# Performance work log

Hardware: AMD Instinct MI355X
Metric: run time of the kernel (lower is better)

The kernel has to match this reference:

```python
import jax, jax.numpy as jnp
import numpy as np

N = 32768          # total nodes
B = 64             # number of graphs (batch.max()+1)
IN_C = 256
OUT_C = 256
NUM_SCALES = 4
NUM_HEADS = 8
BN_EPS = 1e-5


def setup_inputs() -> dict:
    key = jax.random.key(0)
    ks = jax.random.split(key, 10)
    out_s = OUT_C // NUM_SCALES
    x = jax.random.normal(ks[0], (N, IN_C), jnp.float32)
    spectral = jax.random.normal(ks[1], (NUM_SCALES, N, IN_C), jnp.float32)
    batch = jnp.sort(jax.random.randint(ks[2], (N,), 0, B)).astype(jnp.int64)
    # per-scale Linear weights (glorot) and zero biases; stored as [S, in, out_s]
    g = (6.0 / (IN_C + out_s)) ** 0.5
    Ws = jax.random.uniform(ks[3], (NUM_SCALES, IN_C, out_s), jnp.float32, -g, g)
    bs = jnp.zeros((NUM_SCALES, out_s), jnp.float32)
    # MultiheadAttention params (torch layout: in_proj [3E,E], out_proj [E,E])
    s_in = (1.0 / OUT_C) ** 0.5
    W_in = jax.random.uniform(ks[4], (3 * OUT_C, OUT_C), jnp.float32, -s_in, s_in)
    b_in = jnp.zeros((3 * OUT_C,), jnp.float32)
    W_out = jax.random.uniform(ks[5], (OUT_C, OUT_C), jnp.float32, -s_in, s_in)
    b_out = jnp.zeros((OUT_C,), jnp.float32)
    gamma = jnp.ones((OUT_C,), jnp.float32)
    beta = jnp.zeros((OUT_C,), jnp.float32)
    return {"x": x, "spectral": spectral, "Ws": Ws, "bs": bs,
            "W_in": W_in, "b_in": b_in, "W_out": W_out, "b_out": b_out,
            "gamma": gamma, "beta": beta, "batch": batch}


def _forward(x, spectral, Ws, bs, W_in, b_in, W_out, b_out, gamma, beta, batch):
    n, E = x.shape[0], W_out.shape[0]
    # per-scale linear on (x + spectral_feat), concat over scales -> [N, E]
    scale_out = jnp.einsum('sni,sio->sno', x[None] + spectral, Ws) + bs[:, None, :]
    h = jnp.moveaxis(scale_out, 0, 1).reshape(n, E)
    # ragged -> dense padding (batch is sorted segment ids)
    counts = jnp.bincount(batch, length=B)
    max_nodes = int(np.asarray(counts).max())  # data-dependent pad, as in torch
    starts = jnp.concatenate([jnp.zeros((1,), counts.dtype), jnp.cumsum(counts)[:-1]])
    pos = jnp.arange(n) - starts[batch]
    h_pad = jnp.zeros((B, max_nodes, E), h.dtype).at[batch, pos].set(h)
    # MHA over padded graphs (no key-padding mask, matching the source)
    hd = E // NUM_HEADS
    qkv = h_pad @ W_in.T + b_in                       # [B, M, 3E]
    q, k, v = jnp.split(qkv, 3, axis=-1)
    def heads(t):
        return t.reshape(B, max_nodes, NUM_HEADS, hd).transpose(0, 2, 1, 3)
    q, k, v = heads(q) * (hd ** -0.5), heads(k), heads(v)
    attn = jax.nn.softmax(jnp.einsum('bhqd,bhkd->bhqk', q, k), axis=-1)
    ctx = jnp.einsum('bhqk,bhkd->bhqd', attn, v)
    ctx = ctx.transpose(0, 2, 1, 3).reshape(B, max_nodes, E)
    h_att = ctx @ W_out.T + b_out
    # dense -> ragged unpad
    h2 = h_att[batch, pos]                            # [N, E]
    # BatchNorm1d (training-mode batch stats, deterministic) + ReLU; dropout=eval
    mean = h2.mean(axis=0)
    var = h2.var(axis=0)
    hn = (h2 - mean) * jax.lax.rsqrt(var + BN_EPS) * gamma + beta
    return jax.nn.relu(hn)


def reference(x, spectral, Ws, bs, W_in, b_in, W_out, b_out, gamma, beta, batch):
    return _forward(x, spectral, Ws, bs, W_in, b_in, W_out, b_out, gamma, beta, batch)
```

## Files before the change

kernel.cpp:

```cpp
#include <hip/hip_runtime.h>


typedef __attribute__((ext_vector_type(8))) short frag8;
typedef __attribute__((ext_vector_type(4))) short frag4;
typedef __attribute__((ext_vector_type(4))) float f32x4;
typedef __attribute__((ext_vector_type(8))) unsigned short ushort8;
typedef __attribute__((ext_vector_type(2))) unsigned int uint2e;

#define NN 32768
#define NB 64
#define CIN 256
#define COUT 256
#define NHEAD 8
#define HD 32

#define BM 128
#define LDB 264
#define KT 128

#if __has_builtin(__builtin_amdgcn_mfma_f32_16x16x16bf16_1k)
#define HAS_MFMA16 1
#else
#define HAS_MFMA16 0
#endif

__device__ inline unsigned short f2bf(float f) {
  unsigned u = __builtin_bit_cast(unsigned, f);
  u += 0x7FFFu + ((u >> 16) & 1u);
  return (unsigned short)(u >> 16);
}
__device__ inline float bf2f(unsigned short h) {
  return __builtin_bit_cast(float, (unsigned)h << 16);
}
__device__ inline unsigned pack2bf(float a, float b) {
  return (unsigned)f2bf(a) | ((unsigned)f2bf(b) << 16);
}

__global__ void k_prep(const float* __restrict__ Ws, const float* __restrict__ Win,
                       const float* __restrict__ Wout, const int* __restrict__ batch,
                       unsigned short* __restrict__ wst, unsigned short* __restrict__ winb,
                       unsigned short* __restrict__ woutb, int* __restrict__ meta) {
  int tid = blockIdx.x * 256 + threadIdx.x;
  if (tid < NN) {
    int v = batch[tid];
    int prev = (tid == 0) ? -1 : batch[tid - 1];
    for (int bb = prev + 1; bb <= v; ++bb) meta[NB + bb] = tid;
  }
  if (tid < 4 * 64 * 256) {
    int s = tid >> 14, rem = tid & 16383, o = rem >> 8, i = rem & 255;
    wst[tid] = f2bf(Ws[((s * 256) + i) * 64 + o]);
  } else if (tid < 4 * 64 * 256 + 768 * 256) {
    int t2 = tid - 4 * 64 * 256;
    winb[t2] = f2bf(Win[t2]);
  } else if (tid < 4 * 64 * 256 + 768 * 256 + 256 * 256) {
    int t3 = tid - (4 * 64 * 256 + 768 * 256);
    woutb[t3] = f2bf(Wout[t3]);
  }
}
__global__ void k_meta2(int* __restrict__ meta) {
  __shared__ int mx[NB];
  int b = threadIdx.x;
  int s = meta[NB + b];
  int e = (b == 63) ? NN : meta[NB + b + 1];
  meta[b] = e - s;
  mx[b] = e - s;
  __syncthreads();
  if (b == 0) {
    int m = 0;
    for (int j = 0; j < NB; ++j) m = max(m, mx[j]);
    meta[2 * NB] = m;
  }
}

__device__ inline void stage_Bpanel(const unsigned short* __restrict__ Wt,
                                    unsigned short (*Bs)[LDB], int t) {
  int n = t >> 2, seg = t & 3;
  const unsigned short* src = Wt + (size_t)n * 256 + seg * 64;
#pragma unroll
  for (int i = 0; i < 8; ++i) {
    uint4 v = *(const uint4*)(src + i * 8);
    *(uint4*)&Bs[n][seg * 64 + i * 8] = v;
  }
}


__global__ __launch_bounds__(256) void k_scale(const float* __restrict__ x,
                                               const float* __restrict__ spec,
                                               const unsigned short* __restrict__ wst,
                                               const float* __restrict__ bs,
                                               unsigned short* __restrict__ h) {
  __shared__ unsigned short Bs[64][LDB];
  int t = threadIdx.x, lane = t & 63, wave = t >> 6;
  int r0 = blockIdx.x * BM, s = blockIdx.y;
  int m16 = lane & 15, quad = lane >> 4;

  stage_Bpanel(wst + (size_t)s * 64 * 256, Bs, t);
  __syncthreads();

  f32x4 z = {0.f, 0.f, 0.f, 0.f};
  f32x4 acc[2][4];
#pragma unroll
  for (int mi = 0; mi < 2; ++mi)
#pragma unroll
    for (int ni = 0; ni < 4; ++ni) acc[mi][ni] = z;

  const float* sb = spec + (size_t)s * NN * CIN;
#pragma unroll
  for (int kc = 0; kc < 8; ++kc) {
    int kb = kc * 32 + quad * 8;
    frag8 a[2];
#pragma unroll
    for (int mi = 0; mi < 2; ++mi) {
      size_t base = (size_t)(r0 + wave * 32 + mi * 16 + m16) * CIN + kb;
      float4 x0 = *(const float4*)(x + base);
      float4 x1 = *(const float4*)(x + base + 4);
      float4 s0 = *(const float4*)(sb + base);
      float4 s1 = *(const float4*)(sb + base + 4);
      uint4 u;
      u.x = pack2bf(x0.x + s0.x, x0.y + s0.y);
      u.y = pack2bf(x0.z + s0.z, x0.w + s0.w);
      u.z = pack2bf(x1.x + s1.x, x1.y + s1.y);
      u.w = pack2bf(x1.z + s1.z, x1.w + s1.w);
      a[mi] = __builtin_bit_cast(frag8, u);
    }
    frag8 b[4];
#pragma unroll
    for (int ni = 0; ni < 4; ++ni)
      b[ni] = *(const frag8*)&Bs[ni * 16 + m16][kc * 32 + quad * 8];
#pragma unroll
    for (int mi = 0; mi < 2; ++mi)
#pragma unroll
      for (int ni = 0; ni < 4; ++ni)
        acc[mi][ni] = __builtin_amdgcn_mfma_f32_16x16x32_bf16(a[mi], b[ni], acc[mi][ni], 0, 0, 0);
  }

#pragma unroll
  for (int mi = 0; mi < 2; ++mi)
#pragma unroll
    for (int ni = 0; ni < 4; ++ni) {
      int col = ni * 16 + m16;
      float bias = bs[s * 64 + col];
#pragma unroll
      for (int r = 0; r < 4; ++r) {
        int row = r0 + wave * 32 + mi * 16 + quad * 4 + r;
        h[(size_t)row * COUT + s * 64 + col] = f2bf(acc[mi][ni][r] + bias);
      }
    }
}

template <int LDOUT>
__global__ __launch_bounds__(256) void k_lin(const unsigned short* __restrict__ A,
                                             const unsigned short* __restrict__ Wt,
                                             const float* __restrict__ bias,
                                             unsigned short* __restrict__ out) {
  __shared__ unsigned short Bs[64][LDB];
  int t = threadIdx.x, lane = t & 63, wave = t >> 6;
  int r0 = blockIdx.x * BM, c0 = blockIdx.y * 64;
  int m16 = lane & 15, quad = lane >> 4;

  stage_Bpanel(Wt + (size_t)c0 * 256, Bs, t);
  __syncthreads();

  f32x4 z = {0.f, 0.f, 0.f, 0.f};
  f32x4 acc[2][4];
#pragma unroll
  for (int mi = 0; mi < 2; ++mi)
#pragma unroll
    for (int ni = 0; ni < 4; ++ni) acc[mi][ni] = z;

#pragma unroll
  for (int kc = 0; kc < 8; ++kc) {
    int kb = kc * 32 + quad * 8;
    frag8 a[2];
#pragma unroll
    for (int mi = 0; mi < 2; ++mi)
      a[mi] = *(const frag8*)(A + (size_t)(r0 + wave * 32 + mi * 16 + m16) * 256 + kb);
    frag8 b[4];
#pragma unroll
    for (int ni = 0; ni < 4; ++ni)
      b[ni] = *(const frag8*)&Bs[ni * 16 + m16][kc * 32 + quad * 8];
#pragma unroll
    for (int mi = 0; mi < 2; ++mi)
#pragma unroll
      for (int ni = 0; ni < 4; ++ni)
        acc[mi][ni] = __builtin_amdgcn_mfma_f32_16x16x32_bf16(a[mi], b[ni], acc[mi][ni], 0, 0, 0);
  }

#pragma unroll
  for (int mi = 0; mi < 2; ++mi)
#pragma unroll
    for (int ni = 0; ni < 4; ++ni) {
      int col = c0 + ni * 16 + m16;
      float bv = bias[col];
#pragma unroll
      for (int r = 0; r < 4; ++r) {
        int row = r0 + wave * 32 + mi * 16 + quad * 4 + r;
        out[(size_t)row * LDOUT + col] = f2bf(acc[mi][ni][r] + bv);
      }
    }
}

__global__ __launch_bounds__(256) void k_attn_mfma(const unsigned short* __restrict__ qkv,
                                                   const int* __restrict__ meta,
                                                   unsigned short* __restrict__ ctx) {
  int b = blockIdx.x >> 3, head = blockIdx.x & 7;
  int c = meta[b], st = meta[NB + b], M = meta[2 * NB];
  int q0 = blockIdx.y * 128;
  if (q0 >= c) return;

  __shared__ unsigned short Vt[32][KT + 8];

  int t = threadIdx.x, lane = t & 63, wave = t >> 6;
  int m16 = lane & 15, quad = lane >> 4;
  const float SCALE = 0.17677669529663687f;
  float extra = (float)(M - c);

  int qbase = q0 + wave * 32;
  frag8 qf[2];
#pragma unroll
  for (int qg = 0; qg < 2; ++qg) {
    int qrow = qbase + qg * 16 + m16;
    qf[qg] = *(const frag8*)(qkv + (size_t)(st + qrow) * 768 + head * 32 + quad * 8);
  }

  f32x4 zz = {0.f, 0.f, 0.f, 0.f};
  f32x4 O[2][2];
  float lp[2] = {0.f, 0.f};
#pragma unroll
  for (int qg = 0; qg < 2; ++qg) { O[qg][0] = zz; O[qg][1] = zz; }

#if !HAS_MFMA16
  int sl0 = m16 + ((quad & 1) << 5);
  int sl1 = sl0 + 16;
#endif

  for (int kt = 0; kt < c; kt += KT) {
    {
      int key = t >> 1, dh0 = (t & 1) * 16;
      const unsigned short* vp = qkv + (size_t)(st + kt + key) * 768 + 512 + head * 32 + dh0;
      ushort8 v0 = *(const ushort8*)vp;
      ushort8 v1 = *(const ushort8*)(vp + 8);
#pragma unroll
      for (int i = 0; i < 8; ++i) {
        Vt[dh0 + i][key] = v0[i];
        Vt[dh0 + 8 + i][key] = v1[i];
      }
    }
    __syncthreads();

#pragma unroll
    for (int sub = 0; sub < 4; ++sub) {
      int ks = kt + sub * 32;
      if (ks < c) {
        bool full = (ks + 32 <= c);
        frag8 kf[2];
#pragma unroll
        for (int kh = 0; kh < 2; ++kh) {
          int krow = ks + kh * 16 + m16;
          kf[kh] = *(const frag8*)(qkv + (size_t)(st + krow) * 768 + 256 + head * 32 + quad * 8);
        }
        unsigned pk[2][2][2];
#pragma unroll
        for (int qg = 0; qg < 2; ++qg)
#pragma unroll
          for (int kh = 0; kh < 2; ++kh) {
            f32x4 s = __builtin_amdgcn_mfma_f32_16x16x32_bf16(kf[kh], qf[qg], zz, 0, 0, 0);
            float p[4];
#pragma unroll
            for (int r = 0; r < 4; ++r) p[r] = __expf(s[r] * SCALE);
            if (!full) {
#pragma unroll
              for (int r = 0; r < 4; ++r)
                if (ks + kh * 16 + quad * 4 + r >= c) p[r] = 0.f;
            }
            lp[qg] += (p[0] + p[1]) + (p[2] + p[3]);
            pk[qg][kh][0] = pack2bf(p[0], p[1]);
            pk[qg][kh][1] = pack2bf(p[2], p[3]);
          }
#if HAS_MFMA16
        frag4 vb[2][2];
#pragma unroll
        for (int kh = 0; kh < 2; ++kh)
#pragma unroll
          for (int dh = 0; dh < 2; ++dh)
            vb[kh][dh] = *(const frag4*)&Vt[dh * 16 + m16][sub * 32 + kh * 16 + quad * 4];
#pragma unroll
        for (int qg = 0; qg < 2; ++qg) {
          frag4 pa0 = __builtin_bit_cast(frag4, uint2e{pk[qg][0][0], pk[qg][0][1]});
          frag4 pa1 = __builtin_bit_cast(frag4, uint2e{pk[qg][1][0], pk[qg][1][1]});
#pragma unroll
          for (int dh = 0; dh < 2; ++dh) {
            O[qg][dh] = __builtin_amdgcn_mfma_f32_16x16x16bf16_1k(pa0, vb[0][dh], O[qg][dh], 0, 0, 0);
            O[qg][dh] = __builtin_amdgcn_mfma_f32_16x16x16bf16_1k(pa1, vb[1][dh], O[qg][dh], 0, 0, 0);
          }
        }
#else
        frag8 vf[2];
#pragma unroll
        for (int dh = 0; dh < 2; ++dh)
          vf[dh] = *(const frag8*)&Vt[dh * 16 + m16][sub * 32 + quad * 8];
#pragma unroll
        for (int qg = 0; qg < 2; ++qg) {
          unsigned a0 = __shfl(pk[qg][0][0], sl0), a1 = __shfl(pk[qg][0][1], sl0);
          unsigned a2 = __shfl(pk[qg][0][0], sl1), a3 = __shfl(pk[qg][0][1], sl1);
          unsigned b0 = __shfl(pk[qg][1][0], sl0), b1 = __shfl(pk[qg][1][1], sl0);
          unsigned b2 = __shfl(pk[qg][1][0], sl1), b3 = __shfl(pk[qg][1][1], sl1);
          uint4 pw;
          pw.x = (quad < 2) ? a0 : b0;
          pw.y = (quad < 2) ? a1 : b1;
          pw.z = (quad < 2) ? a2 : b2;
          pw.w = (quad < 2) ? a3 : b3;
          frag8 pf = __builtin_bit_cast(frag8, pw);
#pragma unroll
          for (int dh = 0; dh < 2; ++dh)
            O[qg][dh] = __builtin_amdgcn_mfma_f32_16x16x32_bf16(pf, vf[dh], O[qg][dh], 0, 0, 0);
        }
#endif
      }
    }
    __syncthreads();
  }

#pragma unroll
  for (int qg = 0; qg < 2; ++qg) {
    float v = lp[qg];
    v += __shfl_xor(v, 16);
    v += __shfl_xor(v, 32);
    lp[qg] = v;
  }

#pragma unroll
  for (int qg = 0; qg < 2; ++qg)
#pragma unroll
    for (int r = 0; r < 4; ++r) {
      int qrow = qbase + qg * 16 + quad * 4 + r;
      float lsum = __shfl(lp[qg], quad * 4 + r);
      if (qrow < c) {
        float inv = 1.f / (lsum + extra);
        unsigned short* op = ctx + (size_t)(st + qrow) * 256 + head * 32;
        op[m16] = f2bf(O[qg][0][r] * inv);
        op[16 + m16] = f2bf(O[qg][1][r] * inv);
      }
    }
}

__global__ __launch_bounds__(256) void k_stats(const unsigned short* __restrict__ h,
                                               float* __restrict__ sums) {
  int c = threadIdx.x;
  int r0 = blockIdx.x * 64;
  float s = 0.f, s2 = 0.f;
#pragma unroll 8
  for (int r = 0; r < 64; ++r) {
    float v = bf2f(h[(size_t)(r0 + r) * 256 + c]);
    s += v; s2 += v * v;
  }
  atomicAdd(&sums[c], s);
  atomicAdd(&sums[256 + c], s2);
}

__global__ __launch_bounds__(256) void k_bn_apply(const unsigned short* __restrict__ h,
                                                  const float* __restrict__ sums,
                                                  const float* __restrict__ gamma,
                                                  const float* __restrict__ beta,
                                                  float* __restrict__ out) {
  size_t i8 = ((size_t)blockIdx.x * 256 + threadIdx.x) * 8;
  int c0 = (int)(i8 & 255);
  ushort8 v = *(const ushort8*)(h + i8);
  float4 o0, o1;
  float res[8];
#pragma unroll
  for (int i = 0; i < 8; ++i) {
    int ch = c0 + i;
    float mean = sums[ch] * (1.0f / NN);
    float var = sums[256 + ch] * (1.0f / NN) - mean * mean;
    float sc = rsqrtf(var + 1e-5f) * gamma[ch];
    float sh = beta[ch] - mean * sc;
    res[i] = fmaxf(bf2f(v[i]) * sc + sh, 0.f);
  }
  o0.x = res[0]; o0.y = res[1]; o0.z = res[2]; o0.w = res[3];
  o1.x = res[4]; o1.y = res[5]; o1.z = res[6]; o1.w = res[7];
  *(float4*)(out + i8) = o0;
  *(float4*)(out + i8 + 4) = o1;
}

extern "C" void kernel_launch(void* const* d_in, const int* in_sizes, int n_in,
                              void* d_out, int out_size, void* d_ws, size_t ws_size,
                              hipStream_t stream) {
  const float* x      = (const float*)d_in[0];
  const float* spec   = (const float*)d_in[1];
  const float* Ws     = (const float*)d_in[2];
  const float* bs     = (const float*)d_in[3];
  const float* Win    = (const float*)d_in[4];
  const float* b_in   = (const float*)d_in[5];
  const float* Wout   = (const float*)d_in[6];
  const float* b_out  = (const float*)d_in[7];
  const float* gamma  = (const float*)d_in[8];
  const float* beta   = (const float*)d_in[9];
  const int* batch    = (const int*)d_in[10];
  float* out = (float*)d_out;

  char* w = (char*)d_ws;
  size_t off = 0;
  auto alloc = [&](size_t bytes) -> void* {
    off = (off + 255) & ~(size_t)255;
    void* p = w + off; off += bytes; return p;
  };
  int* meta             = (int*)alloc(129 * sizeof(int));
  unsigned short* wst   = (unsigned short*)alloc((size_t)4 * 64 * 256 * 2);
  unsigned short* winb  = (unsigned short*)alloc((size_t)768 * 256 * 2);
  unsigned short* woutb = (unsigned short*)alloc((size_t)256 * 256 * 2);
  float* sums           = (float*)alloc(512 * 4);
  unsigned short* h     = (unsigned short*)alloc((size_t)NN * 256 * 2);
  unsigned short* qkv   = (unsigned short*)alloc((size_t)NN * 768 * 2);
  unsigned short* ctx   = (unsigned short*)alloc((size_t)NN * 256 * 2);
  unsigned short* hatt  = (unsigned short*)alloc((size_t)NN * 256 * 2);

  (void)hipMemsetAsync(sums, 0, 512 * 4, stream);
  k_prep<<<1280, 256, 0, stream>>>(Ws, Win, Wout, batch, wst, winb, woutb, meta);
  k_meta2<<<1, 64, 0, stream>>>(meta);
  k_scale<<<dim3(NN / BM, 4), 256, 0, stream>>>(x, spec, wst, bs, h);
  k_lin<768><<<dim3(NN / BM, 12), 256, 0, stream>>>(h, winb, b_in, qkv);
  k_attn_mfma<<<dim3(NB * NHEAD, 8), 256, 0, stream>>>(qkv, meta, ctx);
  k_lin<256><<<dim3(NN / BM, 4), 256, 0, stream>>>(ctx, woutb, b_out, hatt);
  k_stats<<<NN / 64, 256, 0, stream>>>(hatt, sums);
  k_bn_apply<<<NN * 256 / 2048, 256, 0, stream>>>(hatt, sums, gamma, beta, out);
}
```

Measured before the change: 408.5 us.

## Software-pipeline A-operand loads in GEMM kernels, use hardware bf16 pack and exp2

The scale and linear GEMM kernels now prefetch A-operand global loads three steps ahead through a rotating register ring, hiding load latency behind the MFMA work. Launch bounds are raised to request four blocks per CU. Software bf16 rounding is replaced by the v_cvt_pk_bf16_f32 instruction, and attention softmax uses exp2 with a prescaled constant instead of __expf. The prefetch ring raises register pressure, which may conflict with the occupancy hint.

```diff
diff --git a/kernel.cpp b/kernel.cpp
--- a/kernel.cpp
+++ b/kernel.cpp
@@ -24,6 +24,12 @@
 #define HAS_MFMA16 0
 #endif
 
+#if __has_builtin(__builtin_amdgcn_exp2f)
+#define EXP2(x) __builtin_amdgcn_exp2f(x)
+#else
+#define EXP2(x) __expf((x) * 0.6931471805599453f)
+#endif
+
 __device__ inline unsigned short f2bf(float f) {
   unsigned u = __builtin_bit_cast(unsigned, f);
   u += 0x7FFFu + ((u >> 16) & 1u);
@@ -32,8 +38,10 @@
 __device__ inline float bf2f(unsigned short h) {
   return __builtin_bit_cast(float, (unsigned)h << 16);
 }
-__device__ inline unsigned pack2bf(float a, float b) {
-  return (unsigned)f2bf(a) | ((unsigned)f2bf(b) << 16);
+__device__ inline unsigned cvtpk(float a, float b) {
+  unsigned r;
+  asm("v_cvt_pk_bf16_f32 %0, %1, %2" : "=v"(r) : "v"(a), "v"(b));
+  return r;
 }
 
 __global__ void k_prep(const float* __restrict__ Ws, const float* __restrict__ Win,
@@ -84,17 +92,36 @@
 }
 
 
-__global__ __launch_bounds__(256) void k_scale(const float* __restrict__ x,
-                                               const float* __restrict__ spec,
-                                               const unsigned short* __restrict__ wst,
-                                               const float* __restrict__ bs,
-                                               unsigned short* __restrict__ h) {
+__global__ __launch_bounds__(256, 4) void k_scale(const float* __restrict__ x,
+                                                  const float* __restrict__ spec,
+                                                  const unsigned short* __restrict__ wst,
+                                                  const float* __restrict__ bs,
+                                                  unsigned short* __restrict__ h) {
   __shared__ unsigned short Bs[64][LDB];
   int t = threadIdx.x, lane = t & 63, wave = t >> 6;
   int r0 = blockIdx.x * BM, s = blockIdx.y;
   int m16 = lane & 15, quad = lane >> 4;
 
   stage_Bpanel(wst + (size_t)s * 64 * 256, Bs, t);
+
+  const float* sb = spec + (size_t)s * NN * CIN;
+  size_t rowbase0 = (size_t)(r0 + wave * 32 + m16) * CIN + quad * 8;
+  size_t rowbase1 = rowbase0 + 16 * CIN;
+
+  float4 P[3][4];
+#define ISSUE(slot, kc, mi)                                              \
+  do {                                                                   \
+    size_t base_ = ((mi) ? rowbase1 : rowbase0) + (size_t)(kc) * 32;     \
+    P[(slot)][0] = *(const float4*)(x + base_);                          \
+    P[(slot)][1] = *(const float4*)(x + base_ + 4);                      \
+    P[(slot)][2] = *(const float4*)(sb + base_);                         \
+    P[(slot)][3] = *(const float4*)(sb + base_ + 4);                     \
+  } while (0)
+
+  ISSUE(0, 0, 0);
+  ISSUE(1, 0, 1);
+  ISSUE(2, 1, 0);
+
   __syncthreads();
 
   f32x4 z = {0.f, 0.f, 0.f, 0.f};
@@ -104,35 +131,26 @@
 #pragma unroll
     for (int ni = 0; ni < 4; ++ni) acc[mi][ni] = z;
 
-  const float* sb = spec + (size_t)s * NN * CIN;
-#pragma unroll
-  for (int kc = 0; kc < 8; ++kc) {
-    int kb = kc * 32 + quad * 8;
-    frag8 a[2];
-#pragma unroll
-    for (int mi = 0; mi < 2; ++mi) {
-      size_t base = (size_t)(r0 + wave * 32 + mi * 16 + m16) * CIN + kb;
-      float4 x0 = *(const float4*)(x + base);
-      float4 x1 = *(const float4*)(x + base + 4);
-      float4 s0 = *(const float4*)(sb + base);
-      float4 s1 = *(const float4*)(sb + base + 4);
-      uint4 u;
-      u.x = pack2bf(x0.x + s0.x, x0.y + s0.y);
-      u.y = pack2bf(x0.z + s0.z, x0.w + s0.w);
-      u.z = pack2bf(x1.x + s1.x, x1.y + s1.y);
-      u.w = pack2bf(x1.z + s1.z, x1.w + s1.w);
-      a[mi] = __builtin_bit_cast(frag8, u);
-    }
-    frag8 b[4];
-#pragma unroll
-    for (int ni = 0; ni < 4; ++ni)
-      b[ni] = *(const frag8*)&Bs[ni * 16 + m16][kc * 32 + quad * 8];
-#pragma unroll
-    for (int mi = 0; mi < 2; ++mi)
-#pragma unroll
-      for (int ni = 0; ni < 4; ++ni)
-        acc[mi][ni] = __builtin_amdgcn_mfma_f32_16x16x32_bf16(a[mi], b[ni], acc[mi][ni], 0, 0, 0);
-  }
+#pragma unroll
+  for (int st = 0; st < 16; ++st) {
+    const int kc = st >> 1, mi = st & 1, slot = st % 3;
+    uint4 u;
+    u.x = cvtpk(P[slot][0].x + P[slot][2].x, P[slot][0].y + P[slot][2].y);
+    u.y = cvtpk(P[slot][0].z + P[slot][2].z, P[slot][0].w + P[slot][2].w);
+    u.z = cvtpk(P[slot][1].x + P[slot][3].x, P[slot][1].y + P[slot][3].y);
+    u.w = cvtpk(P[slot][1].z + P[slot][3].z, P[slot][1].w + P[slot][3].w);
+    frag8 a = __builtin_bit_cast(frag8, u);
+    if (st + 3 < 16) ISSUE(slot, (st + 3) >> 1, (st + 3) & 1);
+    frag8 b0 = *(const frag8*)&Bs[m16][kc * 32 + quad * 8];
+    frag8 b1 = *(const frag8*)&Bs[16 + m16][kc * 32 + quad * 8];
+    frag8 b2 = *(const frag8*)&Bs[32 + m16][kc * 32 + quad * 8];
+    frag8 b3 = *(const frag8*)&Bs[48 + m16][kc * 32 + quad * 8];
+    acc[mi][0] = __builtin_amdgcn_mfma_f32_16x16x32_bf16(a, b0, acc[mi][0], 0, 0, 0);
+    acc[mi][1] = __builtin_amdgcn_mfma_f32_16x16x32_bf16(a, b1, acc[mi][1], 0, 0, 0);
+    acc[mi][2] = __builtin_amdgcn_mfma_f32_16x16x32_bf16(a, b2, acc[mi][2], 0, 0, 0);
+    acc[mi][3] = __builtin_amdgcn_mfma_f32_16x16x32_bf16(a, b3, acc[mi][3], 0, 0, 0);
+  }
+#undef ISSUE
 
 #pragma unroll
   for (int mi = 0; mi < 2; ++mi)
@@ -141,24 +159,35 @@
       int col = ni * 16 + m16;
       float bias = bs[s * 64 + col];
 #pragma unroll
-      for (int r = 0; r < 4; ++r) {
-        int row = r0 + wave * 32 + mi * 16 + quad * 4 + r;
-        h[(size_t)row * COUT + s * 64 + col] = f2bf(acc[mi][ni][r] + bias);
+      for (int rp = 0; rp < 2; ++rp) {
+        int row = r0 + wave * 32 + mi * 16 + quad * 4 + rp * 2;
+        unsigned u = cvtpk(acc[mi][ni][rp * 2] + bias, acc[mi][ni][rp * 2 + 1] + bias);
+        h[(size_t)row * COUT + s * 64 + col] = (unsigned short)u;
+        h[(size_t)(row + 1) * COUT + s * 64 + col] = (unsigned short)(u >> 16);
       }
     }
 }
 
 template <int LDOUT>
-__global__ __launch_bounds__(256) void k_lin(const unsigned short* __restrict__ A,
-                                             const unsigned short* __restrict__ Wt,
-                                             const float* __restrict__ bias,
-                                             unsigned short* __restrict__ out) {
+__global__ __launch_bounds__(256, 4) void k_lin(const unsigned short* __restrict__ A,
+                                                const unsigned short* __restrict__ Wt,
+                                                const float* __restrict__ bias,
+                                                unsigned short* __restrict__ out) {
   __shared__ unsigned short Bs[64][LDB];
   int t = threadIdx.x, lane = t & 63, wave = t >> 6;
   int r0 = blockIdx.x * BM, c0 = blockIdx.y * 64;
   int m16 = lane & 15, quad = lane >> 4;
 
   stage_Bpanel(Wt + (size_t)c0 * 256, Bs, t);
+
+  size_t abase0 = (size_t)(r0 + wave * 32 + m16) * 256 + quad * 8;
+  size_t abase1 = abase0 + 16 * 256;
+
+  frag8 PA[3];
+  PA[0] = *(const frag8*)(A + abase0);
+  PA[1] = *(const frag8*)(A + abase1);
+  PA[2] = *(const frag8*)(A + abase0 + 32);
+
   __syncthreads();
 
   f32x4 z = {0.f, 0.f, 0.f, 0.f};
@@ -169,21 +198,21 @@
     for (int ni = 0; ni < 4; ++ni) acc[mi][ni] = z;
 
 #pragma unroll
-  for (int kc = 0; kc < 8; ++kc) {
-    int kb = kc * 32 + quad * 8;
-    frag8 a[2];
-#pragma unroll
-    for (int mi = 0; mi < 2; ++mi)
-      a[mi] = *(const frag8*)(A + (size_t)(r0 + wave * 32 + mi * 16 + m16) * 256 + kb);
-    frag8 b[4];
-#pragma unroll
-    for (int ni = 0; ni < 4; ++ni)
-      b[ni] = *(const frag8*)&Bs[ni * 16 + m16][kc * 32 + quad * 8];
-#pragma unroll
-    for (int mi = 0; mi < 2; ++mi)
-#pragma unroll
-      for (int ni = 0; ni < 4; ++ni)
-        acc[mi][ni] = __builtin_amdgcn_mfma_f32_16x16x32_bf16(a[mi], b[ni], acc[mi][ni], 0, 0, 0);
+  for (int st = 0; st < 16; ++st) {
+    const int kc = st >> 1, mi = st & 1, slot = st % 3;
+    frag8 a = PA[slot];
+    if (st + 3 < 16) {
+      const int nst = st + 3;
+      PA[slot] = *(const frag8*)(A + ((nst & 1) ? abase1 : abase0) + (size_t)(nst >> 1) * 32);
+    }
+    frag8 b0 = *(const frag8*)&Bs[m16][kc * 32 + quad * 8];
+    frag8 b1 = *(const frag8*)&Bs[16 + m16][kc * 32 + quad * 8];
+    frag8 b2 = *(const frag8*)&Bs[32 + m16][kc * 32 + quad * 8];
+    frag8 b3 = *(const frag8*)&Bs[48 + m16][kc * 32 + quad * 8];
+    acc[mi][0] = __builtin_amdgcn_mfma_f32_16x16x32_bf16(a, b0, acc[mi][0], 0, 0, 0);
+    acc[mi][1] = __builtin_amdgcn_mfma_f32_16x16x32_bf16(a, b1, acc[mi][1], 0, 0, 0);
+    acc[mi][2] = __builtin_amdgcn_mfma_f32_16x16x32_bf16(a, b2, acc[mi][2], 0, 0, 0);
+    acc[mi][3] = __builtin_amdgcn_mfma_f32_16x16x32_bf16(a, b3, acc[mi][3], 0, 0, 0);
   }
 
 #pragma unroll
@@ -193,9 +222,11 @@
       int col = c0 + ni * 16 + m16;
       float bv = bias[col];
 #pragma unroll
-      for (int r = 0; r < 4; ++r) {
-        int row = r0 + wave * 32 + mi * 16 + quad * 4 + r;
-        out[(size_t)row * LDOUT + col] = f2bf(acc[mi][ni][r] + bv);
+      for (int rp = 0; rp < 2; ++rp) {
+        int row = r0 + wave * 32 + mi * 16 + quad * 4 + rp * 2;
+        unsigned u = cvtpk(acc[mi][ni][rp * 2] + bv, acc[mi][ni][rp * 2 + 1] + bv);
+        out[(size_t)row * LDOUT + col] = (unsigned short)u;
+        out[(size_t)(row + 1) * LDOUT + col] = (unsigned short)(u >> 16);
       }
     }
 }
@@ -212,7 +243,7 @@
 
   int t = threadIdx.x, lane = t & 63, wave = t >> 6;
   int m16 = lane & 15, quad = lane >> 4;
-  const float SCALE = 0.17677669529663687f;
+  const float SC2 = 0.17677669529663687f * 1.4426950408889634f;
   float extra = (float)(M - c);
 
   int qbase = q0 + wave * 32;
@@ -267,15 +298,15 @@
             f32x4 s = __builtin_amdgcn_mfma_f32_16x16x32_bf16(kf[kh], qf[qg], zz, 0, 0, 0);
             float p[4];
 #pragma unroll
-            for (int r = 0; r < 4; ++r) p[r] = __expf(s[r] * SCALE);
+            for (int r = 0; r < 4; ++r) p[r] = EXP2(s[r] * SC2);
             if (!full) {
 #pragma unroll
               for (int r = 0; r < 4; ++r)
                 if (ks + kh * 16 + quad * 4 + r >= c) p[r] = 0.f;
             }
             lp[qg] += (p[0] + p[1]) + (p[2] + p[3]);
-            pk[qg][kh][0] = pack2bf(p[0], p[1]);
-            pk[qg][kh][1] = pack2bf(p[2], p[3]);
+            pk[qg][kh][0] = cvtpk(p[0], p[1]);
+            pk[qg][kh][1] = cvtpk(p[2], p[3]);
           }
 #if HAS_MFMA16
         frag4 vb[2][2];
@@ -338,8 +369,9 @@
       if (qrow < c) {
         float inv = 1.f / (lsum + extra);
         unsigned short* op = ctx + (size_t)(st + qrow) * 256 + head * 32;
-        op[m16] = f2bf(O[qg][0][r] * inv);
-        op[16 + m16] = f2bf(O[qg][1][r] * inv);
+        unsigned u = cvtpk(O[qg][0][r] * inv, O[qg][1][r] * inv);
+        op[m16] = (unsigned short)u;
+        op[16 + m16] = (unsigned short)(u >> 16);
       }
     }
 }
```

New measurement: 396.8 us. -2.9%, faster.
